# Optimization experiments

Measured on AMD Instinct MI355X. Metric: run time of the kernel, lower is better.

Reference implementation:

```python
import jax, jax.numpy as jnp
import numpy as np

B, LQ, LK, D, H = 2, 1024, 1024, 1024, 16
DH = D // H


def setup_inputs() -> dict:
    key = jax.random.key(0)
    ks = jax.random.split(key, 14)
    s = 1.0 / np.sqrt(D)
    inp = {
        "q": jax.random.normal(ks[0], (B, LQ, D), jnp.float32),
        "k": jax.random.normal(ks[1], (B, LK, D), jnp.float32),
        "v": jax.random.normal(ks[2], (B, LK, D), jnp.float32),
        "Wq": jax.random.normal(ks[3], (D, D), jnp.float32) * s,
        "bq": jnp.zeros((D,), jnp.float32),
        "Wk": jax.random.normal(ks[4], (D, D), jnp.float32) * s,
        "bk": jnp.zeros((D,), jnp.float32),
        "Wv": jax.random.normal(ks[5], (D, D), jnp.float32) * s,
        "bv": jnp.zeros((D,), jnp.float32),
        "Wo": jax.random.normal(ks[6], (D, D), jnp.float32) * s,
        "bo": jnp.zeros((D,), jnp.float32),
        "logits_bias": jax.random.normal(ks[7], (B, LQ, LK), jnp.float32),
        "key_padding_mask": jax.random.randint(ks[8], (B, LK), 0, 2) > 0,
    }
    return inp


def _split_heads(x):
    b, l, _ = x.shape
    return x.reshape(b, l, H, DH).transpose(0, 2, 1, 3)  # [B,H,L,DH]


def reference(q, k, v, Wq, bq, Wk, bk, Wv, bv, Wo, bo, logits_bias, key_padding_mask):
    qh = _split_heads(q @ Wq.T + bq)  # [B,H,Lq,DH]
    kh = _split_heads(k @ Wk.T + bk)  # [B,H,Lk,DH]
    vh = _split_heads(v @ Wv.T + bv)  # [B,H,Lk,DH]

    neg = jnp.finfo(qh.dtype).min
    # attn_mask = logits_bias broadcast over heads, masked_fill at padded keys
    attn_mask = jnp.where(key_padding_mask[:, None, None, :],
                          neg, logits_bias[:, None, :, :])  # [B,1,Lq,Lk]

    scale = 1.0 / np.sqrt(DH)
    scores = jnp.einsum('bhqd,bhkd->bhqk', qh, kh) * scale + attn_mask
    probs = jax.nn.softmax(scores, axis=-1)
    out = jnp.einsum('bhqk,bhkd->bhqd', probs, vh)  # [B,H,Lq,DH]
    out = out.transpose(0, 2, 1, 3).reshape(q.shape[0], q.shape[1], D)
    return out @ Wo.T + bo
```

## Files before the change

### kernel.cpp

```cpp
#include <hip/hip_runtime.h>


typedef _Float16 half8 __attribute__((ext_vector_type(8)));
typedef _Float16 half4_t __attribute__((ext_vector_type(4)));
typedef float f32x4 __attribute__((ext_vector_type(4)));

#define MFMA16(a, b, c) __builtin_amdgcn_mfma_f32_16x16x32_f16((a), (b), (c), 0, 0, 0)

#define WAITCNT_VM(n) asm volatile("s_waitcnt vmcnt(" #n ")" ::: "memory")
#define WAITCNT_LGKM0() asm volatile("s_waitcnt lgkmcnt(0)" ::: "memory")
#define RAW_BARRIER() asm volatile("s_barrier" ::: "memory")
#define EXP2F(x) __builtin_amdgcn_exp2f(x)

__device__ __forceinline__ void gload16(const void* g, void* l) {
  __builtin_amdgcn_global_load_lds(
      (const __attribute__((address_space(1))) unsigned int*)g,
      (__attribute__((address_space(3))) unsigned int*)l, 16, 0, 0);
}

__device__ __forceinline__ half8 frag_ld(const _Float16* t, int row, int ck) {
  return *(const half8*)(t + row * 64 + (((ck ^ (row & 7)) << 3)));
}

__global__ __launch_bounds__(256) void cvt_f32_f16(
    const float* __restrict__ q, const float* __restrict__ k, const float* __restrict__ v,
    const float* __restrict__ Wq, const float* __restrict__ Wk,
    const float* __restrict__ Wv, const float* __restrict__ Wo,
    const float* __restrict__ biasL, const int* __restrict__ kpm,
    _Float16* __restrict__ q16, _Float16* __restrict__ k16, _Float16* __restrict__ v16,
    _Float16* __restrict__ w16, _Float16* __restrict__ biasC) {
  const int y = blockIdx.y;
  if (y == 7) {
    const size_t i = ((size_t)blockIdx.x * 256 + threadIdx.x) * 8;
    const int b = (int)(i >> 20);
    const int kk = (int)(i & 1023);
    const int* mrow = kpm + (b << 10) + kk;
    const float4 b0 = *(const float4*)(biasL + i);
    const float4 b1 = *(const float4*)(biasL + i + 4);
    const int4 m0 = *(const int4*)mrow;
    const int4 m1 = *(const int4*)(mrow + 4);
    const float sc = 1.44269504f;
    half8 h;
    h[0] = m0.x ? (_Float16)-30000.f : (_Float16)(b0.x * sc - 8.f);
    h[1] = m0.y ? (_Float16)-30000.f : (_Float16)(b0.y * sc - 8.f);
    h[2] = m0.z ? (_Float16)-30000.f : (_Float16)(b0.z * sc - 8.f);
    h[3] = m0.w ? (_Float16)-30000.f : (_Float16)(b0.w * sc - 8.f);
    h[4] = m1.x ? (_Float16)-30000.f : (_Float16)(b1.x * sc - 8.f);
    h[5] = m1.y ? (_Float16)-30000.f : (_Float16)(b1.y * sc - 8.f);
    h[6] = m1.z ? (_Float16)-30000.f : (_Float16)(b1.z * sc - 8.f);
    h[7] = m1.w ? (_Float16)-30000.f : (_Float16)(b1.w * sc - 8.f);
    *(half8*)(biasC + i) = h;
    return;
  }
  if (y >= 3 && blockIdx.x >= 512) return;
  const float* s;
  _Float16* d;
  const size_t M = (size_t)1024 * 1024;
  switch (y) {
    case 0: s = q;  d = q16; break;
    case 1: s = k;  d = k16; break;
    case 2: s = v;  d = v16; break;
    case 3: s = Wq; d = w16; break;
    case 4: s = Wk; d = w16 + M; break;
    case 5: s = Wv; d = w16 + 2 * M; break;
    default: s = Wo; d = w16 + 3 * M; break;
  }
  const size_t i = ((size_t)blockIdx.x * 256 + threadIdx.x) * 8;
  const float4 a = *(const float4*)(s + i);
  const float4 bvv = *(const float4*)(s + i + 4);
  half8 h;
  h[0] = (_Float16)a.x; h[1] = (_Float16)a.y; h[2] = (_Float16)a.z; h[3] = (_Float16)a.w;
  h[4] = (_Float16)bvv.x; h[5] = (_Float16)bvv.y; h[6] = (_Float16)bvv.z; h[7] = (_Float16)bvv.w;
  *(half8*)(d + i) = h;
}

__global__ __launch_bounds__(256, 2) void mmp_big(
    const _Float16* __restrict__ Aq, const _Float16* __restrict__ Ak,
    const _Float16* __restrict__ Av, const _Float16* __restrict__ W16,
    const float* __restrict__ c0, const float* __restrict__ c1,
    const float* __restrict__ c2, _Float16* __restrict__ Dq,
    _Float16* __restrict__ Dk, _Float16* __restrict__ Dvt,
    float* __restrict__ Df, int is_final) {
  __shared__ __align__(16) _Float16 lds[32768];

  const int tid = threadIdx.x;
  const int wv = tid >> 6, ln = tid & 63;
  const int quad = ln >> 4, col = ln & 15;
  const int wm = wv >> 1, wn = wv & 1;
  const int n0 = blockIdx.x * 128;
  const int m0 = blockIdx.y * 128;
  const int z = blockIdx.z;
  const bool swapped = is_final || (z < 2);

  const _Float16* A = (z == 0) ? Aq : (z == 1) ? Ak : Av;
  const _Float16* Bw = W16 + (size_t)z * 1024 * 1024;
  const float* bias = (z == 0) ? c0 : (z == 1) ? c1 : c2;

  auto stage = [&](int buf, int k0) {
#pragma unroll
    for (int j = 0; j < 8; ++j) {
      const int ci = j * 256 + tid;
      const _Float16* src;
      if (ci < 1024) {
        const int row = ci >> 3, lc = (ci & 7) ^ (row & 7);
        src = A + (size_t)(m0 + row) * 1024 + k0 + lc * 8;
      } else {
        const int di = ci - 1024;
        const int row = di >> 3, lc = (di & 7) ^ (row & 7);
        src = Bw + (size_t)(n0 + row) * 1024 + k0 + lc * 8;
      }
      gload16(src, lds + buf * 16384 + (j * 256 + wv * 64) * 8);
    }
  };

  const f32x4 zero4 = {0.f, 0.f, 0.f, 0.f};
  f32x4 acc[4][4];
#pragma unroll
  for (int i = 0; i < 4; ++i)
#pragma unroll
    for (int j = 0; j < 4; ++j) acc[i][j] = zero4;

  auto kstep = [&](const _Float16* As, const _Float16* Bs) {
    half8 af0[4], bf0[4], af1[4], bf1[4];
#pragma unroll
    for (int mi = 0; mi < 4; ++mi) af0[mi] = frag_ld(As, wm * 64 + mi * 16 + col, quad);
#pragma unroll
    for (int ni = 0; ni < 4; ++ni) bf0[ni] = frag_ld(Bs, wn * 64 + ni * 16 + col, quad);
#pragma unroll
    for (int mi = 0; mi < 4; ++mi) af1[mi] = frag_ld(As, wm * 64 + mi * 16 + col, 4 + quad);
#pragma unroll
    for (int ni = 0; ni < 4; ++ni) bf1[ni] = frag_ld(Bs, wn * 64 + ni * 16 + col, 4 + quad);
    WAITCNT_LGKM0();
    RAW_BARRIER();
    if (swapped) {
#pragma unroll
      for (int ni = 0; ni < 4; ++ni)
#pragma unroll
        for (int mi = 0; mi < 4; ++mi)
          acc[ni][mi] = MFMA16(bf0[ni], af0[mi], acc[ni][mi]);
#pragma unroll
      for (int ni = 0; ni < 4; ++ni)
#pragma unroll
        for (int mi = 0; mi < 4; ++mi)
          acc[ni][mi] = MFMA16(bf1[ni], af1[mi], acc[ni][mi]);
    } else {
#pragma unroll
      for (int mi = 0; mi < 4; ++mi)
#pragma unroll
        for (int ni = 0; ni < 4; ++ni)
          acc[mi][ni] = MFMA16(af0[mi], bf0[ni], acc[mi][ni]);
#pragma unroll
      for (int mi = 0; mi < 4; ++mi)
#pragma unroll
        for (int ni = 0; ni < 4; ++ni)
          acc[mi][ni] = MFMA16(af1[mi], bf1[ni], acc[mi][ni]);
    }
  };

  stage(0, 0);
  for (int i = 0; i < 15; ++i) {
    stage((i + 1) & 1, (i + 1) * 64);
    WAITCNT_VM(8);
    RAW_BARRIER();
    kstep(lds + (i & 1) * 16384, lds + (i & 1) * 16384 + 8192);
  }
  WAITCNT_VM(0);
  RAW_BARRIER();
  kstep(lds + 16384, lds + 16384 + 8192);

  if (swapped) {
    float4 bv4[4];
#pragma unroll
    for (int ni = 0; ni < 4; ++ni)
      bv4[ni] = *(const float4*)&bias[n0 + wn * 64 + ni * 16 + quad * 4];
    if (is_final) {
#pragma unroll
      for (int ni = 0; ni < 4; ++ni) {
        const int n_g = n0 + wn * 64 + ni * 16 + quad * 4;
#pragma unroll
        for (int mi = 0; mi < 4; ++mi) {
          const int m_g = m0 + wm * 64 + mi * 16 + col;
          float4 st;
          st.x = acc[ni][mi][0] + bv4[ni].x;
          st.y = acc[ni][mi][1] + bv4[ni].y;
          st.z = acc[ni][mi][2] + bv4[ni].z;
          st.w = acc[ni][mi][3] + bv4[ni].w;
          *(float4*)&Df[(size_t)m_g * 1024 + n_g] = st;
        }
      }
    } else {
      _Float16* D = z ? Dk : Dq;
#pragma unroll
      for (int ni = 0; ni < 4; ++ni) {
        const int n_g = n0 + wn * 64 + ni * 16 + quad * 4;
        const int h = n_g >> 6, dh = n_g & 63;
#pragma unroll
        for (int mi = 0; mi < 4; ++mi) {
          const int m_g = m0 + wm * 64 + mi * 16 + col;
          const int b = m_g >> 10, l = m_g & 1023;
          half4_t st;
          st[0] = (_Float16)(acc[ni][mi][0] + bv4[ni].x);
          st[1] = (_Float16)(acc[ni][mi][1] + bv4[ni].y);
          st[2] = (_Float16)(acc[ni][mi][2] + bv4[ni].z);
          st[3] = (_Float16)(acc[ni][mi][3] + bv4[ni].w);
          *(half4_t*)&D[((size_t)((b * 16 + h) * 1024) + l) * 64 + dh] = st;
        }
      }
    }
  } else {
    float bv[4];
#pragma unroll
    for (int ni = 0; ni < 4; ++ni) bv[ni] = bias[n0 + wn * 64 + ni * 16 + col];
    __syncthreads();
    _Float16* Ct = lds;
#pragma unroll
    for (int mi = 0; mi < 4; ++mi) {
      const int ml = wm * 64 + mi * 16 + quad * 4;
#pragma unroll
      for (int ni = 0; ni < 4; ++ni) {
        const int nl = wn * 64 + ni * 16 + col;
        half4_t h;
#pragma unroll
        for (int r = 0; r < 4; ++r) h[r] = (_Float16)(acc[mi][ni][r] + bv[ni]);
        *(half4_t*)(Ct + (size_t)nl * 136 + ml) = h;
      }
    }
    __syncthreads();
#pragma unroll
    for (int it = 0; it < 8; ++it) {
      const int ci = it * 256 + tid;
      const int n = ci >> 4;
      const int mc = (ci & 15) * 8;
      const half8 hv = *(const half8*)(Ct + (size_t)n * 136 + mc);
      const int n_g = n0 + n;
      const int h = n_g >> 6, dh = n_g & 63;
      const int m_g = m0 + mc;
      const int b = m_g >> 10, l = m_g & 1023;
      *(half8*)(Dvt + ((size_t)((b * 16 + h) * 64 + dh)) * 1024 + l) = hv;
    }
  }
}

__global__ __launch_bounds__(512, 4) void attn(
    const _Float16* __restrict__ Qh, const _Float16* __restrict__ Kh,
    const _Float16* __restrict__ Vt, const _Float16* __restrict__ biasC,
    _Float16* __restrict__ AO) {
  __shared__ __align__(16) _Float16 KV[2 * 8192];
  __shared__ __align__(16) _Float16 Pt[8][512];

  const int tid = threadIdx.x;
  const int wv = tid >> 6, ln = tid & 63;
  const int quad = ln >> 4, col = ln & 15;
  const int qsub = wv >> 1, khalf = wv & 1;
  const int q0 = blockIdx.x * 64;
  const int bh = blockIdx.y;
  const int b = bh >> 4, hh = bh & 15;
  const int qg = q0 + qsub * 16 + col;

  const _Float16* Qp = Qh + ((size_t)bh * 1024 + qg) * 64;
  const half8 bq0 = *(const half8*)(Qp + quad * 8);
  const half8 bq1 = *(const half8*)(Qp + 32 + quad * 8);
  WAITCNT_VM(0);

  const _Float16* biasRow = biasC + ((size_t)(b * 1024 + qg)) * 1024;

  auto stageKV = [&](int buf, int it) {
    const int koff = it * 64;
#pragma unroll
    for (int j = 0; j < 2; ++j) {
      const int ci = j * 512 + tid;
      const void* src;
      if (ci < 512) {
        const int row = ci >> 3, lc = (ci & 7) ^ (row & 7);
        src = Kh + ((size_t)bh * 1024 + koff + row) * 64 + lc * 8;
      } else {
        const int di = ci - 512;
        const int row = di >> 3, lc = (di & 7) ^ (row & 7);
        src = Vt + ((size_t)bh * 64 + row) * 1024 + koff + lc * 8;
      }
      gload16(src, KV + buf * 8192 + (j * 512 + wv * 64) * 8);
    }
  };
  auto loadBias = [&](int it, half4_t* bb) {
    const int koff = it * 64 + khalf * 32;
#pragma unroll
    for (int mi = 0; mi < 2; ++mi)
      bb[mi] = *(const half4_t*)&biasRow[koff + mi * 16 + quad * 4];
  };

  const f32x4 zero4 = {0.f, 0.f, 0.f, 0.f};
  f32x4 o[4];
#pragma unroll
  for (int ni = 0; ni < 4; ++ni) o[ni] = zero4;
  float l_i = 0.f;
  _Float16* Pw = Pt[wv];

  auto compute = [&](int buf, const half4_t* bb) {
    const _Float16* Ks = KV + buf * 8192;
    const _Float16* Vs = Ks + 4096;
    f32x4 s[2];
#pragma unroll
    for (int mi = 0; mi < 2; ++mi) {
      f32x4 a4 = zero4;
      a4 = MFMA16(frag_ld(Ks, khalf * 32 + mi * 16 + col, quad), bq0, a4);
      a4 = MFMA16(frag_ld(Ks, khalf * 32 + mi * 16 + col, 4 + quad), bq1, a4);
      s[mi] = a4;
    }
#pragma unroll
    for (int mi = 0; mi < 2; ++mi)
#pragma unroll
      for (int r = 0; r < 4; ++r) {
        const float p = EXP2F(s[mi][r] * 0.18033688f + (float)bb[mi][r]);
        s[mi][r] = p;
        l_i += p;
      }
#pragma unroll
    for (int mi = 0; mi < 2; ++mi) {
      half4_t h;
      h[0] = (_Float16)s[mi][0]; h[1] = (_Float16)s[mi][1];
      h[2] = (_Float16)s[mi][2]; h[3] = (_Float16)s[mi][3];
      const int kloc = mi * 16 + quad * 4;
      *(half4_t*)(Pw + col * 32 + ((((kloc >> 3) ^ (col & 3)) << 3) | (kloc & 7))) = h;
    }
    const half8 p0 = *(const half8*)(Pw + col * 32 + ((quad ^ (col & 3)) << 3));
#pragma unroll
    for (int ni = 0; ni < 4; ++ni)
      o[ni] = MFMA16(frag_ld(Vs, ni * 16 + col, khalf * 4 + quad), p0, o[ni]);
  };

  half4_t bbA[2], bbB[2];
  stageKV(0, 0);
  loadBias(0, bbA);
  for (int i = 0; i < 15; ++i) {
    stageKV((i + 1) & 1, i + 1);
    loadBias(i + 1, bbB);
    WAITCNT_VM(4);
    RAW_BARRIER();
    compute(i & 1, bbA);
    WAITCNT_LGKM0();
    RAW_BARRIER();
    bbA[0] = bbB[0]; bbA[1] = bbB[1];
  }
  WAITCNT_VM(0);
  RAW_BARRIER();
  compute(1, bbA);

  l_i += __shfl_xor(l_i, 16);
  l_i += __shfl_xor(l_i, 32);

  __syncthreads();
  f32x4* Ox = (f32x4*)&KV[0];
  float* MlS = (float*)&KV[8192];
  if (khalf == 1) {
#pragma unroll
    for (int ni = 0; ni < 4; ++ni) Ox[(qsub * 4 + ni) * 64 + ln] = o[ni];
    MlS[qsub * 64 + ln] = l_i;
  }
  __syncthreads();
  if (khalf == 0) {
    const float l2 = MlS[qsub * 64 + ln];
    const float inv = 1.0f / (l_i + l2);
#pragma unroll
    for (int ni = 0; ni < 4; ++ni) {
      const f32x4 o2 = Ox[(qsub * 4 + ni) * 64 + ln];
      half4_t h;
#pragma unroll
      for (int r = 0; r < 4; ++r)
        h[r] = (_Float16)((o[ni][r] + o2[r]) * inv);
      *(half4_t*)&AO[((size_t)(b * 1024 + qg)) * 1024 + hh * 64 + ni * 16 + quad * 4] = h;
    }
  }
}

extern "C" void kernel_launch(void* const* d_in, const int* in_sizes, int n_in,
                              void* d_out, int out_size, void* d_ws, size_t ws_size,
                              hipStream_t stream) {
  (void)in_sizes; (void)n_in; (void)out_size; (void)ws_size;
  const float* q = (const float*)d_in[0];
  const float* k = (const float*)d_in[1];
  const float* v = (const float*)d_in[2];
  const float* Wq = (const float*)d_in[3];
  const float* bq = (const float*)d_in[4];
  const float* Wk = (const float*)d_in[5];
  const float* bk = (const float*)d_in[6];
  const float* Wv = (const float*)d_in[7];
  const float* bv = (const float*)d_in[8];
  const float* Wo = (const float*)d_in[9];
  const float* bo = (const float*)d_in[10];
  const float* lb = (const float*)d_in[11];
  const int* kpm = (const int*)d_in[12];
  float* out = (float*)d_out;

  const size_t NT = (size_t)2 * 1024 * 1024;
  _Float16* q16 = (_Float16*)d_ws;
  _Float16* k16 = q16 + NT;
  _Float16* v16 = k16 + NT;
  _Float16* Qh = v16 + NT;
  _Float16* Kh = Qh + NT;
  _Float16* Vt = Kh + NT;
  _Float16* w16 = Vt + NT;
  _Float16* biasC = w16 + 4 * (NT / 2);
  _Float16* AO = q16;

  cvt_f32_f16<<<dim3(1024, 8), 256, 0, stream>>>(q, k, v, Wq, Wk, Wv, Wo, lb, kpm,
                                                 q16, k16, v16, w16, biasC);
  mmp_big<<<dim3(8, 16, 3), 256, 0, stream>>>(q16, k16, v16, w16, bq, bk, bv,
                                              Qh, Kh, Vt, nullptr, 0);
  attn<<<dim3(16, 32), 512, 0, stream>>>(Qh, Kh, Vt, biasC, AO);
  mmp_big<<<dim3(8, 16, 1), 256, 0, stream>>>(AO, nullptr, nullptr, w16 + 3 * NT / 2,
                                              bo, nullptr, nullptr, nullptr, nullptr,
                                              nullptr, out, 1);
}
```

Baseline: 170.6 us.

## Split output projection into smaller-tile kernel, remap attention blocks by XCD, pack conversion grid

Adds a dedicated output-projection GEMM that uses 64x128 tiles, which doubles the block count from 128 to 256 so more CUs are filled. The attention grid becomes 1D and is remapped so that blocks on the same XCD (fid&7) handle the same batch-head groups, aiming for better L2 reuse of K/V. The conversion kernel folds the four weight conversions into two grid rows so no blocks exit idle. The risks are a smaller per-block reuse ratio in the final GEMM and a mapping that depends on round-robin XCD dispatch.

```diff
diff --git a/kernel.cpp b/kernel.cpp
--- a/kernel.cpp
+++ b/kernel.cpp
@@ -30,7 +30,7 @@
     _Float16* __restrict__ q16, _Float16* __restrict__ k16, _Float16* __restrict__ v16,
     _Float16* __restrict__ w16, _Float16* __restrict__ biasC) {
   const int y = blockIdx.y;
-  if (y == 7) {
+  if (y == 5) {
     const size_t i = ((size_t)blockIdx.x * 256 + threadIdx.x) * 8;
     const int b = (int)(i >> 20);
     const int kk = (int)(i & 1023);
@@ -52,20 +52,18 @@
     *(half8*)(biasC + i) = h;
     return;
   }
-  if (y >= 3 && blockIdx.x >= 512) return;
   const float* s;
   _Float16* d;
   const size_t M = (size_t)1024 * 1024;
+  int x = blockIdx.x;
   switch (y) {
     case 0: s = q;  d = q16; break;
     case 1: s = k;  d = k16; break;
     case 2: s = v;  d = v16; break;
-    case 3: s = Wq; d = w16; break;
-    case 4: s = Wk; d = w16 + M; break;
-    case 5: s = Wv; d = w16 + 2 * M; break;
-    default: s = Wo; d = w16 + 3 * M; break;
-  }
-  const size_t i = ((size_t)blockIdx.x * 256 + threadIdx.x) * 8;
+    case 3: if (x < 512) { s = Wq; d = w16; } else { s = Wk; d = w16 + M; x -= 512; } break;
+    default: if (x < 512) { s = Wv; d = w16 + 2 * M; } else { s = Wo; d = w16 + 3 * M; x -= 512; } break;
+  }
+  const size_t i = ((size_t)x * 256 + threadIdx.x) * 8;
   const float4 a = *(const float4*)(s + i);
   const float4 bvv = *(const float4*)(s + i + 4);
   half8 h;
@@ -79,8 +77,7 @@
     const _Float16* __restrict__ Av, const _Float16* __restrict__ W16,
     const float* __restrict__ c0, const float* __restrict__ c1,
     const float* __restrict__ c2, _Float16* __restrict__ Dq,
-    _Float16* __restrict__ Dk, _Float16* __restrict__ Dvt,
-    float* __restrict__ Df, int is_final) {
+    _Float16* __restrict__ Dk, _Float16* __restrict__ Dvt) {
   __shared__ __align__(16) _Float16 lds[32768];
 
   const int tid = threadIdx.x;
@@ -90,7 +87,7 @@
   const int n0 = blockIdx.x * 128;
   const int m0 = blockIdx.y * 128;
   const int z = blockIdx.z;
-  const bool swapped = is_final || (z < 2);
+  const bool swapped = (z < 2);
 
   const _Float16* A = (z == 0) ? Aq : (z == 1) ? Ak : Av;
   const _Float16* Bw = W16 + (size_t)z * 1024 * 1024;
@@ -173,38 +170,21 @@
 #pragma unroll
     for (int ni = 0; ni < 4; ++ni)
       bv4[ni] = *(const float4*)&bias[n0 + wn * 64 + ni * 16 + quad * 4];
-    if (is_final) {
-#pragma unroll
-      for (int ni = 0; ni < 4; ++ni) {
-        const int n_g = n0 + wn * 64 + ni * 16 + quad * 4;
-#pragma unroll
-        for (int mi = 0; mi < 4; ++mi) {
-          const int m_g = m0 + wm * 64 + mi * 16 + col;
-          float4 st;
-          st.x = acc[ni][mi][0] + bv4[ni].x;
-          st.y = acc[ni][mi][1] + bv4[ni].y;
-          st.z = acc[ni][mi][2] + bv4[ni].z;
-          st.w = acc[ni][mi][3] + bv4[ni].w;
-          *(float4*)&Df[(size_t)m_g * 1024 + n_g] = st;
-        }
-      }
-    } else {
-      _Float16* D = z ? Dk : Dq;
-#pragma unroll
-      for (int ni = 0; ni < 4; ++ni) {
-        const int n_g = n0 + wn * 64 + ni * 16 + quad * 4;
-        const int h = n_g >> 6, dh = n_g & 63;
-#pragma unroll
-        for (int mi = 0; mi < 4; ++mi) {
-          const int m_g = m0 + wm * 64 + mi * 16 + col;
-          const int b = m_g >> 10, l = m_g & 1023;
-          half4_t st;
-          st[0] = (_Float16)(acc[ni][mi][0] + bv4[ni].x);
-          st[1] = (_Float16)(acc[ni][mi][1] + bv4[ni].y);
-          st[2] = (_Float16)(acc[ni][mi][2] + bv4[ni].z);
-          st[3] = (_Float16)(acc[ni][mi][3] + bv4[ni].w);
-          *(half4_t*)&D[((size_t)((b * 16 + h) * 1024) + l) * 64 + dh] = st;
-        }
+    _Float16* D = z ? Dk : Dq;
+#pragma unroll
+    for (int ni = 0; ni < 4; ++ni) {
+      const int n_g = n0 + wn * 64 + ni * 16 + quad * 4;
+      const int h = n_g >> 6, dh = n_g & 63;
+#pragma unroll
+      for (int mi = 0; mi < 4; ++mi) {
+        const int m_g = m0 + wm * 64 + mi * 16 + col;
+        const int b = m_g >> 10, l = m_g & 1023;
+        half4_t st;
+        st[0] = (_Float16)(acc[ni][mi][0] + bv4[ni].x);
+        st[1] = (_Float16)(acc[ni][mi][1] + bv4[ni].y);
+        st[2] = (_Float16)(acc[ni][mi][2] + bv4[ni].z);
+        st[3] = (_Float16)(acc[ni][mi][3] + bv4[ni].w);
+        *(half4_t*)&D[((size_t)((b * 16 + h) * 1024) + l) * 64 + dh] = st;
       }
     }
   } else {
@@ -241,6 +221,95 @@
   }
 }
 
+__global__ __launch_bounds__(256) void mmp_final(
+    const _Float16* __restrict__ A, const _Float16* __restrict__ Bw,
+    const float* __restrict__ bias, float* __restrict__ Df) {
+  __shared__ __align__(16) _Float16 lds[24576];
+
+  const int tid = threadIdx.x;
+  const int wv = tid >> 6, ln = tid & 63;
+  const int quad = ln >> 4, col = ln & 15;
+  const int wm = wv >> 1, wn = wv & 1;
+  const int n0 = blockIdx.x * 128;
+  const int m0 = blockIdx.y * 64;
+
+  auto stage = [&](int buf, int k0) {
+#pragma unroll
+    for (int j = 0; j < 6; ++j) {
+      const int ci = j * 256 + tid;
+      const _Float16* src;
+      if (ci < 512) {
+        const int row = ci >> 3, lc = (ci & 7) ^ (row & 7);
+        src = A + (size_t)(m0 + row) * 1024 + k0 + lc * 8;
+      } else {
+        const int di = ci - 512;
+        const int row = di >> 3, lc = (di & 7) ^ (row & 7);
+        src = Bw + (size_t)(n0 + row) * 1024 + k0 + lc * 8;
+      }
+      gload16(src, lds + buf * 12288 + (j * 256 + wv * 64) * 8);
+    }
+  };
+
+  const f32x4 zero4 = {0.f, 0.f, 0.f, 0.f};
+  f32x4 acc[4][2];
+#pragma unroll
+  for (int i = 0; i < 4; ++i)
+#pragma unroll
+    for (int j = 0; j < 2; ++j) acc[i][j] = zero4;
+
+  auto kstep = [&](const _Float16* As, const _Float16* Bs) {
+    half8 af[2][2], bf[2][4];
+#pragma unroll
+    for (int kk = 0; kk < 2; ++kk) {
+#pragma unroll
+      for (int mi = 0; mi < 2; ++mi)
+        af[kk][mi] = frag_ld(As, wm * 32 + mi * 16 + col, kk * 4 + quad);
+#pragma unroll
+      for (int ni = 0; ni < 4; ++ni)
+        bf[kk][ni] = frag_ld(Bs, wn * 64 + ni * 16 + col, kk * 4 + quad);
+    }
+    WAITCNT_LGKM0();
+    RAW_BARRIER();
+#pragma unroll
+    for (int kk = 0; kk < 2; ++kk)
+#pragma unroll
+      for (int ni = 0; ni < 4; ++ni)
+#pragma unroll
+        for (int mi = 0; mi < 2; ++mi)
+          acc[ni][mi] = MFMA16(bf[kk][ni], af[kk][mi], acc[ni][mi]);
+  };
+
+  stage(0, 0);
+  for (int i = 0; i < 15; ++i) {
+    stage((i + 1) & 1, (i + 1) * 64);
+    WAITCNT_VM(6);
+    RAW_BARRIER();
+    kstep(lds + (i & 1) * 12288, lds + (i & 1) * 12288 + 4096);
+  }
+  WAITCNT_VM(0);
+  RAW_BARRIER();
+  kstep(lds + 12288, lds + 12288 + 4096);
+
+  float4 bv4[4];
+#pragma unroll
+  for (int ni = 0; ni < 4; ++ni)
+    bv4[ni] = *(const float4*)&bias[n0 + wn * 64 + ni * 16 + quad * 4];
+#pragma unroll
+  for (int ni = 0; ni < 4; ++ni) {
+    const int n_g = n0 + wn * 64 + ni * 16 + quad * 4;
+#pragma unroll
+    for (int mi = 0; mi < 2; ++mi) {
+      const int m_g = m0 + wm * 32 + mi * 16 + col;
+      float4 st;
+      st.x = acc[ni][mi][0] + bv4[ni].x;
+      st.y = acc[ni][mi][1] + bv4[ni].y;
+      st.z = acc[ni][mi][2] + bv4[ni].z;
+      st.w = acc[ni][mi][3] + bv4[ni].w;
+      *(float4*)&Df[(size_t)m_g * 1024 + n_g] = st;
+    }
+  }
+}
+
 __global__ __launch_bounds__(512, 4) void attn(
     const _Float16* __restrict__ Qh, const _Float16* __restrict__ Kh,
     const _Float16* __restrict__ Vt, const _Float16* __restrict__ biasC,
@@ -252,8 +321,10 @@
   const int wv = tid >> 6, ln = tid & 63;
   const int quad = ln >> 4, col = ln & 15;
   const int qsub = wv >> 1, khalf = wv & 1;
-  const int q0 = blockIdx.x * 64;
-  const int bh = blockIdx.y;
+  const int fid = blockIdx.x;
+  const int xcd = fid & 7, g = fid >> 3;
+  const int bh = (xcd << 2) | (g >> 4);
+  const int q0 = (g & 15) * 64;
   const int b = bh >> 4, hh = bh & 15;
   const int qg = q0 + qsub * 16 + col;
 
@@ -402,12 +473,10 @@
   _Float16* biasC = w16 + 4 * (NT / 2);
   _Float16* AO = q16;
 
-  cvt_f32_f16<<<dim3(1024, 8), 256, 0, stream>>>(q, k, v, Wq, Wk, Wv, Wo, lb, kpm,
+  cvt_f32_f16<<<dim3(1024, 6), 256, 0, stream>>>(q, k, v, Wq, Wk, Wv, Wo, lb, kpm,
                                                  q16, k16, v16, w16, biasC);
   mmp_big<<<dim3(8, 16, 3), 256, 0, stream>>>(q16, k16, v16, w16, bq, bk, bv,
-                                              Qh, Kh, Vt, nullptr, 0);
-  attn<<<dim3(16, 32), 512, 0, stream>>>(Qh, Kh, Vt, biasC, AO);
-  mmp_big<<<dim3(8, 16, 1), 256, 0, stream>>>(AO, nullptr, nullptr, w16 + 3 * NT / 2,
-                                              bo, nullptr, nullptr, nullptr, nullptr,
-                                              nullptr, out, 1);
-}
+                                              Qh, Kh, Vt);
+  attn<<<dim3(512), 512, 0, stream>>>(Qh, Kh, Vt, biasC, AO);
+  mmp_final<<<dim3(8, 32), 256, 0, stream>>>(AO, w16 + 3 * NT / 2, bo, out);
+}
```

Result: faster. 167.1 us (-2.1%).
